# Kernel tuning notes

Hardware: AMD Instinct MI355X
Metric: run time of the kernel (lower is better)

The kernel has to match this reference:

```python
import jax, jax.numpy as jnp
import numpy as np

B, L = 64, 512          # graphs, nodes per graph
N = B * L               # total nodes
INPUT_DIM, D, H, LAYERS, OUT = 128, 128, 8, 6, 10
DH = D // H
FF = 4 * D
E = 4 * N
SCALE = 0.02


def setup_inputs() -> dict:
    key = jax.random.key(0)
    ks = jax.random.split(key, 12)
    p = {}
    p['x'] = jax.random.normal(ks[0], (N, INPUT_DIM), jnp.float32)
    p['edge_index'] = jax.random.randint(ks[1], (2, E), 0, N, dtype=jnp.int64)
    p['batch'] = jnp.repeat(jnp.arange(B, dtype=jnp.int32), L)  # sorted graph ids
    p['max_nodes'] = L
    p['Wp'] = jax.random.normal(ks[2], (INPUT_DIM, D), jnp.float32) * SCALE
    p['bp'] = jnp.zeros((D,), jnp.float32)
    p['qkv_w'] = jax.random.normal(ks[3], (LAYERS, 3 * D, D), jnp.float32) * SCALE
    p['qkv_b'] = jnp.zeros((LAYERS, 3 * D), jnp.float32)
    p['out_w'] = jax.random.normal(ks[4], (LAYERS, D, D), jnp.float32) * SCALE
    p['out_b'] = jnp.zeros((LAYERS, D), jnp.float32)
    p['ln1_g'] = jnp.ones((LAYERS, D), jnp.float32)
    p['ln1_b'] = jnp.zeros((LAYERS, D), jnp.float32)
    p['ffn_w1'] = jax.random.normal(ks[5], (LAYERS, D, FF), jnp.float32) * SCALE
    p['ffn_b1'] = jnp.zeros((LAYERS, FF), jnp.float32)
    p['ffn_w2'] = jax.random.normal(ks[6], (LAYERS, FF, D), jnp.float32) * SCALE
    p['ffn_b2'] = jnp.zeros((LAYERS, D), jnp.float32)
    p['ln2_g'] = jnp.ones((LAYERS, D), jnp.float32)
    p['ln2_b'] = jnp.zeros((LAYERS, D), jnp.float32)
    p['cls_w1'] = jax.random.normal(ks[7], (D, D // 2), jnp.float32) * SCALE
    p['cls_b1'] = jnp.zeros((D // 2,), jnp.float32)
    p['cls_w2'] = jax.random.normal(ks[8], (D // 2, OUT), jnp.float32) * SCALE
    p['cls_b2'] = jnp.zeros((OUT,), jnp.float32)
    return p


def _ln(x, g, b, eps=1e-5):
    m = x.mean(-1, keepdims=True)
    v = ((x - m) ** 2).mean(-1, keepdims=True)
    return (x - m) * jax.lax.rsqrt(v + eps) * g + b


def _forward(x, batch, max_nodes, Wp, bp, qkv_w, qkv_b, out_w, out_b,
             ln1_g, ln1_b, ffn_w1, ffn_b1, ffn_w2, ffn_b2, ln2_g, ln2_b,
             cls_w1, cls_b1, cls_w2, cls_b2):
    n = x.shape[0]
    # --- vectorized ragged-to-dense (replaces the per-graph python loop) ---
    ones = jnp.ones((n,), jnp.int32)
    counts = jax.ops.segment_sum(ones, batch, num_segments=B)          # [B]
    starts = jnp.concatenate([jnp.zeros((1,), jnp.int32), jnp.cumsum(counts)[:-1]])
    pos = jnp.arange(n, dtype=jnp.int32) - starts[batch]               # slot within graph
    h0 = x @ Wp + bp                                                   # [N, D]
    h = jnp.zeros((B, max_nodes, D), h0.dtype).at[batch, pos].set(h0)  # [B, L, D]
    mask = jnp.zeros((B, max_nodes), bool).at[batch, pos].set(True)    # [B, L]
    # additive key-padding bias (src_key_padding_mask=~mask)
    bias = jnp.where(mask, 0.0, -1e9)[:, None, None, :]                # [B,1,1,L]
    inv_sqrt = 1.0 / np.sqrt(DH)
    for i in range(LAYERS):
        # --- post-norm MHA block ---
        qkv = jnp.einsum('bld,ed->ble', h, qkv_w[i]) + qkv_b[i]        # [B,L,3D]
        q, k, v = jnp.split(qkv, 3, axis=-1)
        q = q.reshape(B, max_nodes, H, DH).transpose(0, 2, 1, 3)       # [B,H,L,dh]
        k = k.reshape(B, max_nodes, H, DH).transpose(0, 2, 1, 3)
        v = v.reshape(B, max_nodes, H, DH).transpose(0, 2, 1, 3)
        scores = jnp.einsum('bhqd,bhkd->bhqk', q, k) * inv_sqrt + bias
        attn = jax.nn.softmax(scores, axis=-1)
        o = jnp.einsum('bhqk,bhkd->bhqd', attn, v)                     # [B,H,L,dh]
        o = o.transpose(0, 2, 1, 3).reshape(B, max_nodes, D)
        o = jnp.einsum('bld,ed->ble', o, out_w[i]) + out_b[i]
        h = _ln(h + o, ln1_g[i], ln1_b[i])
        # --- FFN block ---
        ff = jax.nn.relu(h @ ffn_w1[i] + ffn_b1[i]) @ ffn_w2[i] + ffn_b2[i]
        h = _ln(h + ff, ln2_g[i], ln2_b[i])
    # --- masked mean pooling per graph ---
    denom = jnp.maximum(counts.astype(h.dtype), 1.0)[:, None]          # [B,1]
    pooled = (h * mask[..., None].astype(h.dtype)).sum(axis=1) / denom # [B,D]
    # --- classifier head ---
    hid = jax.nn.relu(pooled @ cls_w1 + cls_b1)
    return hid @ cls_w2 + cls_b2                                       # [B,OUT]


def reference(x, edge_index, batch, max_nodes, Wp, bp, qkv_w, qkv_b, out_w, out_b,
              ln1_g, ln1_b, ffn_w1, ffn_b1, ffn_w2, ffn_b2, ln2_g, ln2_b,
              cls_w1, cls_b1, cls_w2, cls_b2):
    # edge_index is accepted (as in the torch module) but never used.
    return _forward(x, batch, max_nodes, Wp, bp, qkv_w, qkv_b, out_w, out_b,
                    ln1_g, ln1_b, ffn_w1, ffn_b1, ffn_w2, ffn_b2, ln2_g, ln2_b,
                    cls_w1, cls_b1, cls_w2, cls_b2)
```

## Files before the change

kernel.cpp:

```cpp
#include <hip/hip_runtime.h>
#include <hip/hip_bf16.h>


#define NROWS (64 * 512)
#define NLAYER 6

typedef __bf16 bf16x8 __attribute__((ext_vector_type(8)));
typedef float  f32x4  __attribute__((ext_vector_type(4)));
typedef float  f32x16 __attribute__((ext_vector_type(16)));

#define QSCALE 0.36067376022224085f

#if defined(__has_builtin)
#  if __has_builtin(__builtin_amdgcn_exp2f)
#    define FAST_EXP2(x) __builtin_amdgcn_exp2f(x)
#  endif
#endif
#ifndef FAST_EXP2
#  define FAST_EXP2(x) __expf((x) * 0.6931471805599453f)
#endif

__device__ __forceinline__ __hip_bfloat16 f2bf(float x) { return __float2bfloat16(x); }

__device__ __forceinline__ __hip_bfloat16 bf_rta(float a) {
  union { float f; unsigned u; } c{a};
  return __builtin_bit_cast(__hip_bfloat16, (unsigned short)((c.u + 0x8000u) >> 16));
}
__device__ __forceinline__ unsigned pk_rta(float a, float b) {
  union { float f; unsigned u; } ca{a}, cb{b};
  return ((ca.u + 0x8000u) >> 16) | ((cb.u + 0x8000u) & 0xFFFF0000u);
}

#define PN_X   (NROWS * 128)
#define PN_WP  (128 * 128)
#define PN_QW  (6 * 384 * 128)
#define PN_QB  (6 * 384)
#define PN_OW  (6 * 128 * 128)
#define PN_W1  (6 * 128 * 512)
#define PN_W2  (6 * 512 * 128)
#define PB1 PN_X
#define PB2 (PB1 + PN_WP)
#define PB3 (PB2 + PN_QW)
#define PB4 (PB3 + PN_QB)
#define PB5 (PB4 + PN_OW)
#define PB6 (PB5 + PN_W1)
#define PB7 (PB6 + PN_W2)

__global__ __launch_bounds__(256) void prep_kernel(
    const float* __restrict__ x, __hip_bfloat16* __restrict__ xb,
    const float* __restrict__ Wp, __hip_bfloat16* __restrict__ wp_t,
    const float* __restrict__ qkv_w, __hip_bfloat16* __restrict__ qkvw,
    const float* __restrict__ qkv_b, float* __restrict__ qb_s,
    const float* __restrict__ out_w, __hip_bfloat16* __restrict__ outw,
    const float* __restrict__ ffn_w1, __hip_bfloat16* __restrict__ w1t,
    const float* __restrict__ ffn_w2, __hip_bfloat16* __restrict__ w2t)
{
  const int idx = blockIdx.x * 256 + threadIdx.x;
  if (idx < PB1) {
    xb[idx] = f2bf(x[idx]);
  } else if (idx < PB2) {
    const int i = idx - PB1;
    const int c = i >> 7, r = i & 127;
    wp_t[i] = f2bf(Wp[r * 128 + c]);
  } else if (idx < PB3) {
    const int i = idx - PB2;
    const int row = (i >> 7) % 384;
    qkvw[i] = f2bf(qkv_w[i] * ((row < 128) ? QSCALE : 1.f));
  } else if (idx < PB4) {
    const int i = idx - PB3;
    qb_s[i] = qkv_b[i] * (((i % 384) < 128) ? QSCALE : 1.f);
  } else if (idx < PB5) {
    const int i = idx - PB4;
    outw[i] = f2bf(out_w[i]);
  } else if (idx < PB6) {
    const int i = idx - PB5;
    const int l = i >> 16, j = i & 65535;
    const int c = j >> 7, r = j & 127;
    w1t[i] = f2bf(ffn_w1[l * 65536 + r * 512 + c]);
  } else if (idx < PB7) {
    const int i = idx - PB6;
    const int l = i >> 16, j = i & 65535;
    const int c = j >> 9, r = j & 511;
    w2t[i] = f2bf(ffn_w2[l * 65536 + r * 128 + c]);
  }
}

__global__ __launch_bounds__(256) void gemm_fk(
    const __hip_bfloat16* __restrict__ A, const __hip_bfloat16* __restrict__ B,
    const float* __restrict__ bias, __hip_bfloat16* __restrict__ outb,
    __hip_bfloat16* __restrict__ hb,
    const float* __restrict__ lng, const float* __restrict__ lnb,
    int M, int K, int flags)
{
  __shared__ __align__(16) __hip_bfloat16 As[64 * 136];
  __shared__ __align__(16) __hip_bfloat16 Bs[128 * 136];

  const int tid = threadIdx.x;
  const int m0 = blockIdx.x << 6;
  const int wave = tid >> 6;
  const int lane = tid & 63;
  const int quad = lane >> 4;
  const int l15 = lane & 15;
  const int wrow = wave * 16;

  f32x4 acc[8];
#pragma unroll
  for (int ni = 0; ni < 8; ++ni) acc[ni] = (f32x4){0.f, 0.f, 0.f, 0.f};

  for (int kc = 0; kc < K; kc += 128) {
#pragma unroll
    for (int p = 0; p < 4; ++p) {
      const int e = tid + (p << 8);
      const int row = e >> 4;
      const int c = e & 15;
      *(uint4*)&As[row * 136 + c * 8] =
          *(const uint4*)(A + (size_t)(m0 + row) * K + kc + c * 8);
    }
#pragma unroll
    for (int p = 0; p < 8; ++p) {
      const int e = tid + (p << 8);
      const int row = e >> 4;
      const int c = e & 15;
      *(uint4*)&Bs[row * 136 + c * 8] =
          *(const uint4*)(B + (size_t)row * K + kc + c * 8);
    }
    __syncthreads();

#pragma unroll
    for (int ks = 0; ks < 4; ++ks) {
      const bf16x8 af = *(const bf16x8*)&As[(wrow + l15) * 136 + ks * 32 + quad * 8];
#pragma unroll
      for (int ni = 0; ni < 8; ++ni) {
        const bf16x8 bfr =
            *(const bf16x8*)&Bs[(ni * 16 + l15) * 136 + ks * 32 + quad * 8];
        acc[ni] = __builtin_amdgcn_mfma_f32_16x16x32_bf16(af, bfr, acc[ni], 0, 0, 0);
      }
    }
    if (kc + 128 < K) __syncthreads();
  }

  if (flags & 2) {
#pragma unroll
    for (int r = 0; r < 4; ++r) {
      const size_t row = (size_t)(m0 + wrow + quad * 4 + r);
      float s = 0.f, sq = 0.f;
#pragma unroll
      for (int ni = 0; ni < 8; ++ni) {
        const int cl = ni * 16 + l15;
        const float v = acc[ni][r] + bias[cl] +
                        __bfloat162float(hb[row * 128 + cl]);
        acc[ni][r] = v;
        s += v;
        sq += v * v;
      }
#pragma unroll
      for (int off = 1; off <= 8; off <<= 1) {
        s += __shfl_xor(s, off, 64);
        sq += __shfl_xor(sq, off, 64);
      }
      const float mean = s * (1.f / 128.f);
      const float var = sq * (1.f / 128.f) - mean * mean;
      const float rs = rsqrtf(var + 1e-5f);
#pragma unroll
      for (int ni = 0; ni < 8; ++ni) {
        const int cl = ni * 16 + l15;
        const float o = (acc[ni][r] - mean) * rs * lng[cl] + lnb[cl];
        hb[row * 128 + cl] = bf_rta(o);
      }
    }
  } else {
#pragma unroll
    for (int ni = 0; ni < 8; ++ni) {
      const int cl = ni * 16 + l15;
      const float bv = bias[cl];
#pragma unroll
      for (int r = 0; r < 4; ++r) {
        float v = acc[ni][r] + bv;
        if (flags & 1) v = fmaxf(v, 0.f);
        outb[(size_t)(m0 + wrow + quad * 4 + r) * 128 + cl] = bf_rta(v);
      }
    }
  }
}

__global__ __launch_bounds__(256) void ffn_fused(
    __hip_bfloat16* __restrict__ hb,
    const __hip_bfloat16* __restrict__ w1,
    const __hip_bfloat16* __restrict__ w2,
    const float* __restrict__ b1, const float* __restrict__ b2,
    const float* __restrict__ lng, const float* __restrict__ lnb)
{
  __shared__ __align__(16) __hip_bfloat16 AF[64 * 136];
  __shared__ __align__(16) __hip_bfloat16 Bs[128 * 136];

  const int tid = threadIdx.x;
  const int m0 = blockIdx.x << 6;
  const int wave = tid >> 6;
  const int lane = tid & 63;
  const int quad = lane >> 4;
  const int l15 = lane & 15;
  const int wrow = wave * 16;

#pragma unroll
  for (int p = 0; p < 4; ++p) {
    const int e = tid + (p << 8);
    const int row = e >> 4, c = e & 15;
    *(uint4*)&AF[row * 136 + c * 8] =
        *(const uint4*)(hb + (size_t)(m0 + row) * 128 + c * 8);
  }
#pragma unroll
  for (int p = 0; p < 8; ++p) {
    const int e = tid + (p << 8);
    const int row = e >> 4, c = e & 15;
    *(uint4*)&Bs[row * 136 + c * 8] =
        *(const uint4*)(w1 + (size_t)row * 128 + c * 8);
  }
  __syncthreads();

  bf16x8 af[4];
#pragma unroll
  for (int ks = 0; ks < 4; ++ks)
    af[ks] = *(const bf16x8*)&AF[(wrow + l15) * 136 + ks * 32 + quad * 8];

  f32x4 oacc[8];
#pragma unroll
  for (int ni = 0; ni < 8; ++ni) oacc[ni] = (f32x4){0.f, 0.f, 0.f, 0.f};

  for (int c = 0; c < 4; ++c) {
    if (c > 0) {
      __syncthreads();
#pragma unroll
      for (int p = 0; p < 8; ++p) {
        const int e = tid + (p << 8);
        const int row = e >> 4, cc = e & 15;
        *(uint4*)&Bs[row * 136 + cc * 8] =
            *(const uint4*)(w1 + (size_t)(c * 128 + row) * 128 + cc * 8);
      }
      __syncthreads();
    }

    f32x4 fc[8];
#pragma unroll
    for (int ni = 0; ni < 8; ++ni) fc[ni] = (f32x4){0.f, 0.f, 0.f, 0.f};
#pragma unroll
    for (int ks = 0; ks < 4; ++ks)
#pragma unroll
      for (int ni = 0; ni < 8; ++ni) {
        const bf16x8 wf =
            *(const bf16x8*)&Bs[(ni * 16 + l15) * 136 + ks * 32 + quad * 8];
        fc[ni] = __builtin_amdgcn_mfma_f32_16x16x32_bf16(wf, af[ks], fc[ni], 0, 0, 0);
      }
#pragma unroll
    for (int ni = 0; ni < 8; ++ni) {
      const f32x4 bv = *(const f32x4*)(b1 + c * 128 + ni * 16 + quad * 4);
      const float v0 = fmaxf(fc[ni][0] + bv[0], 0.f);
      const float v1 = fmaxf(fc[ni][1] + bv[1], 0.f);
      const float v2 = fmaxf(fc[ni][2] + bv[2], 0.f);
      const float v3 = fmaxf(fc[ni][3] + bv[3], 0.f);
      *(uint2*)&AF[(wrow + l15) * 136 + ni * 16 + quad * 4] =
          make_uint2(pk_rta(v0, v1), pk_rta(v2, v3));
    }
    __syncthreads();

#pragma unroll
    for (int p = 0; p < 8; ++p) {
      const int e = tid + (p << 8);
      const int row = e >> 4, cc = e & 15;
      *(uint4*)&Bs[row * 136 + cc * 8] =
          *(const uint4*)(w2 + (size_t)row * 512 + c * 128 + cc * 8);
    }
    __syncthreads();

#pragma unroll
    for (int ks2 = 0; ks2 < 4; ++ks2) {
      const bf16x8 ff =
          *(const bf16x8*)&AF[(wrow + l15) * 136 + ks2 * 32 + quad * 8];
#pragma unroll
      for (int ni = 0; ni < 8; ++ni) {
        const bf16x8 wf =
            *(const bf16x8*)&Bs[(ni * 16 + l15) * 136 + ks2 * 32 + quad * 8];
        oacc[ni] = __builtin_amdgcn_mfma_f32_16x16x32_bf16(ff, wf, oacc[ni], 0, 0, 0);
      }
    }
  }

#pragma unroll
  for (int r = 0; r < 4; ++r) {
    const size_t row = (size_t)(m0 + wrow + quad * 4 + r);
    float s = 0.f, sq = 0.f;
#pragma unroll
    for (int ni = 0; ni < 8; ++ni) {
      const int cl = ni * 16 + l15;
      const float v = oacc[ni][r] + b2[cl] + __bfloat162float(hb[row * 128 + cl]);
      oacc[ni][r] = v;
      s += v;
      sq += v * v;
    }
#pragma unroll
    for (int off = 1; off <= 8; off <<= 1) {
      s += __shfl_xor(s, off, 64);
      sq += __shfl_xor(sq, off, 64);
    }
    const float mean = s * (1.f / 128.f);
    const float var = sq * (1.f / 128.f) - mean * mean;
    const float rs = rsqrtf(var + 1e-5f);
#pragma unroll
    for (int ni = 0; ni < 8; ++ni) {
      const int cl = ni * 16 + l15;
      const float o = (oacc[ni][r] - mean) * rs * lng[cl] + lnb[cl];
      hb[row * 128 + cl] = bf_rta(o);
    }
  }
}

__global__ __launch_bounds__(512) void attn_kernel(
    const __hip_bfloat16* __restrict__ hbf,
    const __hip_bfloat16* __restrict__ qkvw_l,
    const float* __restrict__ qb_l,
    __hip_bfloat16* __restrict__ o)
{
  __shared__ __align__(16) __hip_bfloat16 Ks[512 * 24];
  __shared__ __align__(16) __hip_bfloat16 Vt[16 * 520];
  __shared__ __align__(16) __hip_bfloat16 PQ[8][1536];

  const int tid = threadIdx.x;
  const int b = blockIdx.x & 63;
  const int hh = blockIdx.x >> 6;
  const __hip_bfloat16* hrow = hbf + (size_t)b * 512 * 128;

  const int wave = tid >> 6;
  const int lane = tid & 63;
  const int l31 = lane & 31;
  const int l5 = lane >> 5;
  const int l15 = lane & 15;
  const int quad = lane >> 4;
  const int q0 = wave * 64;

  {
    f32x4 qacc[4], kacc[4], vacc[4];
#pragma unroll
    for (int mt = 0; mt < 4; ++mt) {
      qacc[mt] = (f32x4){0.f, 0.f, 0.f, 0.f};
      kacc[mt] = (f32x4){0.f, 0.f, 0.f, 0.f};
      vacc[mt] = (f32x4){0.f, 0.f, 0.f, 0.f};
    }
#pragma unroll
    for (int ks = 0; ks < 4; ++ks) {
      const int kc = ks * 32 + quad * 8;
      const bf16x8 wq = *(const bf16x8*)(qkvw_l + (size_t)(hh * 16 + l15) * 128 + kc);
      const bf16x8 wk = *(const bf16x8*)(qkvw_l + (size_t)(128 + hh * 16 + l15) * 128 + kc);
      const bf16x8 wv = *(const bf16x8*)(qkvw_l + (size_t)(256 + hh * 16 + l15) * 128 + kc);
#pragma unroll
      for (int mt = 0; mt < 4; ++mt) {
        const bf16x8 hf =
            *(const bf16x8*)(hrow + (size_t)(q0 + mt * 16 + l15) * 128 + kc);
        qacc[mt] = __builtin_amdgcn_mfma_f32_16x16x32_bf16(hf, wq, qacc[mt], 0, 0, 0);
        kacc[mt] = __builtin_amdgcn_mfma_f32_16x16x32_bf16(hf, wk, kacc[mt], 0, 0, 0);
        vacc[mt] = __builtin_amdgcn_mfma_f32_16x16x32_bf16(wv, hf, vacc[mt], 0, 0, 0);
      }
    }
    const float qb = qb_l[hh * 16 + l15];
    const float kb = qb_l[128 + hh * 16 + l15];
    const f32x4 vb = *(const f32x4*)(qb_l + 256 + hh * 16 + quad * 4);
#pragma unroll
    for (int mt = 0; mt < 4; ++mt)
#pragma unroll
      for (int r = 0; r < 4; ++r) {
        const int nd = mt * 16 + quad * 4 + r;
        PQ[wave][nd * 24 + l15] = bf_rta(qacc[mt][r] + qb);
        Ks[(q0 + nd) * 24 + l15] = bf_rta(kacc[mt][r] + kb);
        Vt[(quad * 4 + r) * 520 + q0 + mt * 16 + l15] = bf_rta(vacc[mt][r] + vb[r]);
      }
  }

  bf16x8 qf[2];
#pragma unroll
  for (int s = 0; s < 2; ++s)
    qf[s] = *(const bf16x8*)&PQ[wave][(s * 32 + l31) * 24 + l5 * 8];
  __syncthreads();

  __hip_bfloat16* Pw = &PQ[wave][0];
  const f32x16 z16 = {};
  f32x4 oacc[2][2];
#pragma unroll
  for (int s = 0; s < 2; ++s) { oacc[s][0] = (f32x4){0.f,0.f,0.f,0.f};
                                oacc[s][1] = (f32x4){0.f,0.f,0.f,0.f}; }
  float lacc[2] = {0.f, 0.f};

  for (int kt = 0; kt < 16; ++kt) {
    const bf16x8 kf = *(const bf16x8*)&Ks[(kt * 32 + l31) * 24 + l5 * 8];
    const bf16x8 vf = *(const bf16x8*)&Vt[l15 * 520 + kt * 32 + quad * 8];
#pragma unroll
    for (int s = 0; s < 2; ++s) {
      f32x16 st = __builtin_amdgcn_mfma_f32_32x32x16_bf16(kf, qf[s], z16, 0, 0, 0);
      float pr[16];
#pragma unroll
      for (int r = 0; r < 16; ++r) pr[r] = FAST_EXP2(st[r]);
      const float s0 = (pr[0] + pr[1]) + (pr[2] + pr[3]);
      const float s1 = (pr[4] + pr[5]) + (pr[6] + pr[7]);
      const float s2 = (pr[8] + pr[9]) + (pr[10] + pr[11]);
      const float s3 = (pr[12] + pr[13]) + (pr[14] + pr[15]);
      lacc[s] += (s0 + s1) + (s2 + s3);
#pragma unroll
      for (int g = 0; g < 4; ++g) {
        *(uint2*)&Pw[l31 * 40 + g * 8 + l5 * 4] =
            make_uint2(pk_rta(pr[g * 4 + 0], pr[g * 4 + 1]),
                       pk_rta(pr[g * 4 + 2], pr[g * 4 + 3]));
      }
#pragma unroll
      for (int g = 0; g < 2; ++g) {
        const bf16x8 pf = *(const bf16x8*)&Pw[(g * 16 + l15) * 40 + quad * 8];
        oacc[s][g] = __builtin_amdgcn_mfma_f32_16x16x32_bf16(vf, pf, oacc[s][g], 0, 0, 0);
      }
    }
  }

#pragma unroll
  for (int s = 0; s < 2; ++s) {
    const float lv = lacc[s] + __shfl_xor(lacc[s], 32, 64);
#pragma unroll
    for (int g = 0; g < 2; ++g) {
      const float lq = __shfl(lv, g * 16 + l15, 64);
      const float inv = 1.f / lq;
      const int qrow = q0 + s * 32 + g * 16 + l15;
      *(uint2*)(o + ((size_t)b * 512 + qrow) * 128 + hh * 16 + quad * 4) =
          make_uint2(pk_rta(oacc[s][g][0] * inv, oacc[s][g][1] * inv),
                     pk_rta(oacc[s][g][2] * inv, oacc[s][g][3] * inv));
    }
  }
}

__global__ __launch_bounds__(256) void head_kernel(
    const __hip_bfloat16* __restrict__ h,
    const float* __restrict__ w1, const float* __restrict__ b1,
    const float* __restrict__ w2, const float* __restrict__ b2,
    float* __restrict__ out)
{
  __shared__ float part[2][128];
  __shared__ float pooled[128];
  __shared__ float hid[64];

  const int b = blockIdx.x;
  const int tid = threadIdx.x;
  const int d = tid & 127;
  const int half = tid >> 7;

  const __hip_bfloat16* hp = h + ((size_t)b * 512 + (size_t)half * 256) * 128;
  float s = 0.f;
  for (int r = 0; r < 256; ++r) s += __bfloat162float(hp[(size_t)r * 128 + d]);
  part[half][d] = s;
  __syncthreads();

  if (tid < 128) pooled[tid] = (part[0][tid] + part[1][tid]) * (1.f / 512.f);
  __syncthreads();

  if (tid < 64) {
    float a = b1[tid];
    for (int dd = 0; dd < 128; ++dd) a = fmaf(pooled[dd], w1[dd * 64 + tid], a);
    hid[tid] = fmaxf(a, 0.f);
  }
  __syncthreads();

  if (tid < 10) {
    float a = b2[tid];
    for (int j = 0; j < 64; ++j) a = fmaf(hid[j], w2[j * 10 + tid], a);
    out[b * 10 + tid] = a;
  }
}

extern "C" void kernel_launch(void* const* d_in, const int* in_sizes, int n_in,
                              void* d_out, int out_size, void* d_ws, size_t ws_size,
                              hipStream_t stream)
{
  (void)in_sizes; (void)n_in; (void)out_size; (void)ws_size;

  const float* x      = (const float*)d_in[0];
  const float* Wp     = (const float*)d_in[4];
  const float* bp     = (const float*)d_in[5];
  const float* qkv_w  = (const float*)d_in[6];
  const float* qkv_b  = (const float*)d_in[7];
  const float* out_w  = (const float*)d_in[8];
  const float* out_b  = (const float*)d_in[9];
  const float* ln1_g  = (const float*)d_in[10];
  const float* ln1_b  = (const float*)d_in[11];
  const float* ffn_w1 = (const float*)d_in[12];
  const float* ffn_b1 = (const float*)d_in[13];
  const float* ffn_w2 = (const float*)d_in[14];
  const float* ffn_b2 = (const float*)d_in[15];
  const float* ln2_g  = (const float*)d_in[16];
  const float* ln2_b  = (const float*)d_in[17];
  const float* cw1    = (const float*)d_in[18];
  const float* cb1    = (const float*)d_in[19];
  const float* cw2    = (const float*)d_in[20];
  const float* cb2    = (const float*)d_in[21];

  const int N = NROWS;

  __hip_bfloat16* hbf   = (__hip_bfloat16*)d_ws;
  __hip_bfloat16* xb    = hbf + (size_t)N * 128;
  __hip_bfloat16* attnb = xb + (size_t)N * 128;
  __hip_bfloat16* wp_t  = attnb + (size_t)N * 128;
  __hip_bfloat16* qkvw  = wp_t + 128 * 128;
  __hip_bfloat16* outw  = qkvw + 6 * 384 * 128;
  __hip_bfloat16* w1t   = outw + 6 * 128 * 128;
  __hip_bfloat16* w2t   = w1t + 6 * 512 * 128;
  float* qb_s = (float*)(w2t + 6 * 128 * 512);

  const dim3 blk(256);
  __hip_bfloat16* const nob = (__hip_bfloat16*)nullptr;
  const float* const nof = (const float*)nullptr;

  prep_kernel<<<dim3((PB7 + 255) / 256), blk, 0, stream>>>(
      x, xb, Wp, wp_t, qkv_w, qkvw, qkv_b, qb_s, out_w, outw,
      ffn_w1, w1t, ffn_w2, w2t);

  gemm_fk<<<dim3(N / 64), blk, 0, stream>>>(
      xb, wp_t, bp, hbf, nob, nof, nof, N, 128, 0);

  for (int i = 0; i < NLAYER; ++i) {
    attn_kernel<<<dim3(64 * 8), dim3(512), 0, stream>>>(
        hbf, qkvw + (size_t)i * 384 * 128, qb_s + (size_t)i * 384, attnb);

    gemm_fk<<<dim3(N / 64), blk, 0, stream>>>(
        attnb, outw + (size_t)i * 128 * 128, out_b + (size_t)i * 128,
        nob, hbf, ln1_g + (size_t)i * 128, ln1_b + (size_t)i * 128,
        N, 128, 2);

    ffn_fused<<<dim3(N / 64), blk, 0, stream>>>(
        hbf, w1t + (size_t)i * 512 * 128, w2t + (size_t)i * 128 * 512,
        ffn_b1 + (size_t)i * 512, ffn_b2 + (size_t)i * 128,
        ln2_g + (size_t)i * 128, ln2_b + (size_t)i * 128);
  }

  head_kernel<<<dim3(64), blk, 0, stream>>>(hbf, cw1, cb1, cw2, cb2, (float*)d_out);
}
```

Before: 511.8 us.

## Fuse out-projection+LN1 into FFN kernel and transpose MFMA operand order

Merges the attention output projection, residual add and first LayerNorm into the FFN kernel, so each layer runs one block kernel instead of two. The LN1 result stays in registers and shared memory as the FFN input and residual, which removes one global write and read of the hidden state per layer and one launch. MFMA operand order is swapped so each lane holds 4 contiguous columns of a row. That allows vectorized bias/gamma loads and packed stores in both the block kernel and the QKV projection in attention. The cost is a longer kernel with more live registers (hnew plus accumulators), which may lower occupancy.

New measurement: 600.2 us. 1.17x slower.

```diff
diff --git a/kernel.cpp b/kernel.cpp
--- a/kernel.cpp
+++ b/kernel.cpp
@@ -88,9 +88,7 @@
 __global__ __launch_bounds__(256) void gemm_fk(
     const __hip_bfloat16* __restrict__ A, const __hip_bfloat16* __restrict__ B,
     const float* __restrict__ bias, __hip_bfloat16* __restrict__ outb,
-    __hip_bfloat16* __restrict__ hb,
-    const float* __restrict__ lng, const float* __restrict__ lnb,
-    int M, int K, int flags)
+    int M, int K)
 {
   __shared__ __align__(16) __hip_bfloat16 As[64 * 136];
   __shared__ __align__(16) __hip_bfloat16 Bs[128 * 136];
@@ -139,56 +137,26 @@
     if (kc + 128 < K) __syncthreads();
   }
 
-  if (flags & 2) {
-#pragma unroll
-    for (int r = 0; r < 4; ++r) {
-      const size_t row = (size_t)(m0 + wrow + quad * 4 + r);
-      float s = 0.f, sq = 0.f;
-#pragma unroll
-      for (int ni = 0; ni < 8; ++ni) {
-        const int cl = ni * 16 + l15;
-        const float v = acc[ni][r] + bias[cl] +
-                        __bfloat162float(hb[row * 128 + cl]);
-        acc[ni][r] = v;
-        s += v;
-        sq += v * v;
-      }
-#pragma unroll
-      for (int off = 1; off <= 8; off <<= 1) {
-        s += __shfl_xor(s, off, 64);
-        sq += __shfl_xor(sq, off, 64);
-      }
-      const float mean = s * (1.f / 128.f);
-      const float var = sq * (1.f / 128.f) - mean * mean;
-      const float rs = rsqrtf(var + 1e-5f);
-#pragma unroll
-      for (int ni = 0; ni < 8; ++ni) {
-        const int cl = ni * 16 + l15;
-        const float o = (acc[ni][r] - mean) * rs * lng[cl] + lnb[cl];
-        hb[row * 128 + cl] = bf_rta(o);
-      }
-    }
-  } else {
-#pragma unroll
-    for (int ni = 0; ni < 8; ++ni) {
-      const int cl = ni * 16 + l15;
-      const float bv = bias[cl];
-#pragma unroll
-      for (int r = 0; r < 4; ++r) {
-        float v = acc[ni][r] + bv;
-        if (flags & 1) v = fmaxf(v, 0.f);
-        outb[(size_t)(m0 + wrow + quad * 4 + r) * 128 + cl] = bf_rta(v);
-      }
-    }
-  }
-}
-
-__global__ __launch_bounds__(256) void ffn_fused(
+#pragma unroll
+  for (int ni = 0; ni < 8; ++ni) {
+    const int cl = ni * 16 + l15;
+    const float bv = bias[cl];
+#pragma unroll
+    for (int r = 0; r < 4; ++r)
+      outb[(size_t)(m0 + wrow + quad * 4 + r) * 128 + cl] = bf_rta(acc[ni][r] + bv);
+  }
+}
+
+__global__ __launch_bounds__(256) void block_kernel(
+    const __hip_bfloat16* __restrict__ attnb,
     __hip_bfloat16* __restrict__ hb,
+    const __hip_bfloat16* __restrict__ outw,
+    const float* __restrict__ out_b,
+    const float* __restrict__ ln1_g, const float* __restrict__ ln1_b,
     const __hip_bfloat16* __restrict__ w1,
     const __hip_bfloat16* __restrict__ w2,
     const float* __restrict__ b1, const float* __restrict__ b2,
-    const float* __restrict__ lng, const float* __restrict__ lnb)
+    const float* __restrict__ ln2_g, const float* __restrict__ ln2_b)
 {
   __shared__ __align__(16) __hip_bfloat16 AF[64 * 136];
   __shared__ __align__(16) __hip_bfloat16 Bs[128 * 136];
@@ -199,45 +167,94 @@
   const int lane = tid & 63;
   const int quad = lane >> 4;
   const int l15 = lane & 15;
-  const int wrow = wave * 16;
+  const int lrow = wave * 16 + l15;
+  const size_t grow = (size_t)(m0 + lrow);
 
 #pragma unroll
   for (int p = 0; p < 4; ++p) {
     const int e = tid + (p << 8);
     const int row = e >> 4, c = e & 15;
     *(uint4*)&AF[row * 136 + c * 8] =
-        *(const uint4*)(hb + (size_t)(m0 + row) * 128 + c * 8);
+        *(const uint4*)(attnb + (size_t)(m0 + row) * 128 + c * 8);
   }
 #pragma unroll
   for (int p = 0; p < 8; ++p) {
     const int e = tid + (p << 8);
     const int row = e >> 4, c = e & 15;
     *(uint4*)&Bs[row * 136 + c * 8] =
-        *(const uint4*)(w1 + (size_t)row * 128 + c * 8);
+        *(const uint4*)(outw + (size_t)row * 128 + c * 8);
   }
   __syncthreads();
 
   bf16x8 af[4];
 #pragma unroll
   for (int ks = 0; ks < 4; ++ks)
-    af[ks] = *(const bf16x8*)&AF[(wrow + l15) * 136 + ks * 32 + quad * 8];
-
-  f32x4 oacc[8];
-#pragma unroll
-  for (int ni = 0; ni < 8; ++ni) oacc[ni] = (f32x4){0.f, 0.f, 0.f, 0.f};
+    af[ks] = *(const bf16x8*)&AF[lrow * 136 + ks * 32 + quad * 8];
+
+  f32x4 acc[8];
+#pragma unroll
+  for (int ni = 0; ni < 8; ++ni) acc[ni] = (f32x4){0.f, 0.f, 0.f, 0.f};
+#pragma unroll
+  for (int ks = 0; ks < 4; ++ks)
+#pragma unroll
+    for (int ni = 0; ni < 8; ++ni) {
+      const bf16x8 bfr =
+          *(const bf16x8*)&Bs[(ni * 16 + l15) * 136 + ks * 32 + quad * 8];
+      acc[ni] = __builtin_amdgcn_mfma_f32_16x16x32_bf16(bfr, af[ks], acc[ni], 0, 0, 0);
+    }
+
+  f32x4 hnew[8];
+  {
+    float s = 0.f, sq = 0.f;
+#pragma unroll
+    for (int ni = 0; ni < 8; ++ni) {
+      const f32x4 bv = *(const f32x4*)(out_b + ni * 16 + quad * 4);
+      const uint2 ru = *(const uint2*)(hb + grow * 128 + ni * 16 + quad * 4);
+      const __hip_bfloat16* rh = (const __hip_bfloat16*)&ru;
+#pragma unroll
+      for (int r = 0; r < 4; ++r) {
+        const float v = acc[ni][r] + bv[r] + __bfloat162float(rh[r]);
+        hnew[ni][r] = v;
+        s += v;
+        sq += v * v;
+      }
+    }
+    s += __shfl_xor(s, 16, 64);  sq += __shfl_xor(sq, 16, 64);
+    s += __shfl_xor(s, 32, 64);  sq += __shfl_xor(sq, 32, 64);
+    const float mean = s * (1.f / 128.f);
+    const float var = sq * (1.f / 128.f) - mean * mean;
+    const float rs = rsqrtf(var + 1e-5f);
+#pragma unroll
+    for (int ni = 0; ni < 8; ++ni) {
+      const f32x4 g4 = *(const f32x4*)(ln1_g + ni * 16 + quad * 4);
+      const f32x4 b4 = *(const f32x4*)(ln1_b + ni * 16 + quad * 4);
+      f32x4 o;
+#pragma unroll
+      for (int r = 0; r < 4; ++r) o[r] = (hnew[ni][r] - mean) * rs * g4[r] + b4[r];
+      hnew[ni] = o;
+      *(uint2*)&AF[lrow * 136 + ni * 16 + quad * 4] =
+          make_uint2(pk_rta(o[0], o[1]), pk_rta(o[2], o[3]));
+    }
+  }
+
+  bf16x8 af2[4];
+#pragma unroll
+  for (int ks = 0; ks < 4; ++ks)
+    af2[ks] = *(const bf16x8*)&AF[lrow * 136 + ks * 32 + quad * 8];
+
+#pragma unroll
+  for (int ni = 0; ni < 8; ++ni) acc[ni] = (f32x4){0.f, 0.f, 0.f, 0.f};
 
   for (int c = 0; c < 4; ++c) {
-    if (c > 0) {
-      __syncthreads();
-#pragma unroll
-      for (int p = 0; p < 8; ++p) {
-        const int e = tid + (p << 8);
-        const int row = e >> 4, cc = e & 15;
-        *(uint4*)&Bs[row * 136 + cc * 8] =
-            *(const uint4*)(w1 + (size_t)(c * 128 + row) * 128 + cc * 8);
-      }
-      __syncthreads();
-    }
+    __syncthreads();
+#pragma unroll
+    for (int p = 0; p < 8; ++p) {
+      const int e = tid + (p << 8);
+      const int row = e >> 4, cc = e & 15;
+      *(uint4*)&Bs[row * 136 + cc * 8] =
+          *(const uint4*)(w1 + (size_t)(c * 128 + row) * 128 + cc * 8);
+    }
+    __syncthreads();
 
     f32x4 fc[8];
 #pragma unroll
@@ -248,7 +265,7 @@
       for (int ni = 0; ni < 8; ++ni) {
         const bf16x8 wf =
             *(const bf16x8*)&Bs[(ni * 16 + l15) * 136 + ks * 32 + quad * 8];
-        fc[ni] = __builtin_amdgcn_mfma_f32_16x16x32_bf16(wf, af[ks], fc[ni], 0, 0, 0);
+        fc[ni] = __builtin_amdgcn_mfma_f32_16x16x32_bf16(wf, af2[ks], fc[ni], 0, 0, 0);
       }
 #pragma unroll
     for (int ni = 0; ni < 8; ++ni) {
@@ -257,11 +274,10 @@
       const float v1 = fmaxf(fc[ni][1] + bv[1], 0.f);
       const float v2 = fmaxf(fc[ni][2] + bv[2], 0.f);
       const float v3 = fmaxf(fc[ni][3] + bv[3], 0.f);
-      *(uint2*)&AF[(wrow + l15) * 136 + ni * 16 + quad * 4] =
+      *(uint2*)&AF[lrow * 136 + ni * 16 + quad * 4] =
           make_uint2(pk_rta(v0, v1), pk_rta(v2, v3));
     }
     __syncthreads();
-
 #pragma unroll
     for (int p = 0; p < 8; ++p) {
       const int e = tid + (p << 8);
@@ -273,42 +289,44 @@
 
 #pragma unroll
     for (int ks2 = 0; ks2 < 4; ++ks2) {
-      const bf16x8 ff =
-          *(const bf16x8*)&AF[(wrow + l15) * 136 + ks2 * 32 + quad * 8];
+      const bf16x8 ff = *(const bf16x8*)&AF[lrow * 136 + ks2 * 32 + quad * 8];
 #pragma unroll
       for (int ni = 0; ni < 8; ++ni) {
         const bf16x8 wf =
             *(const bf16x8*)&Bs[(ni * 16 + l15) * 136 + ks2 * 32 + quad * 8];
-        oacc[ni] = __builtin_amdgcn_mfma_f32_16x16x32_bf16(ff, wf, oacc[ni], 0, 0, 0);
-      }
-    }
-  }
-
-#pragma unroll
-  for (int r = 0; r < 4; ++r) {
-    const size_t row = (size_t)(m0 + wrow + quad * 4 + r);
+        acc[ni] = __builtin_amdgcn_mfma_f32_16x16x32_bf16(wf, ff, acc[ni], 0, 0, 0);
+      }
+    }
+  }
+
+  {
     float s = 0.f, sq = 0.f;
 #pragma unroll
     for (int ni = 0; ni < 8; ++ni) {
-      const int cl = ni * 16 + l15;
-      const float v = oacc[ni][r] + b2[cl] + __bfloat162float(hb[row * 128 + cl]);
-      oacc[ni][r] = v;
-      s += v;
-      sq += v * v;
-    }
-#pragma unroll
-    for (int off = 1; off <= 8; off <<= 1) {
-      s += __shfl_xor(s, off, 64);
-      sq += __shfl_xor(sq, off, 64);
-    }
+      const f32x4 bv = *(const f32x4*)(b2 + ni * 16 + quad * 4);
+#pragma unroll
+      for (int r = 0; r < 4; ++r) {
+        const float v = acc[ni][r] + bv[r] + hnew[ni][r];
+        acc[ni][r] = v;
+        s += v;
+        sq += v * v;
+      }
+    }
+    s += __shfl_xor(s, 16, 64);  sq += __shfl_xor(sq, 16, 64);
+    s += __shfl_xor(s, 32, 64);  sq += __shfl_xor(sq, 32, 64);
     const float mean = s * (1.f / 128.f);
     const float var = sq * (1.f / 128.f) - mean * mean;
     const float rs = rsqrtf(var + 1e-5f);
 #pragma unroll
     for (int ni = 0; ni < 8; ++ni) {
-      const int cl = ni * 16 + l15;
-      const float o = (oacc[ni][r] - mean) * rs * lng[cl] + lnb[cl];
-      hb[row * 128 + cl] = bf_rta(o);
+      const f32x4 g4 = *(const f32x4*)(ln2_g + ni * 16 + quad * 4);
+      const f32x4 b4 = *(const f32x4*)(ln2_b + ni * 16 + quad * 4);
+      const float o0 = (acc[ni][0] - mean) * rs * g4[0] + b4[0];
+      const float o1 = (acc[ni][1] - mean) * rs * g4[1] + b4[1];
+      const float o2 = (acc[ni][2] - mean) * rs * g4[2] + b4[2];
+      const float o3 = (acc[ni][3] - mean) * rs * g4[3] + b4[3];
+      *(uint2*)(hb + grow * 128 + ni * 16 + quad * 4) =
+          make_uint2(pk_rta(o0, o1), pk_rta(o2, o3));
     }
   }
 }
@@ -354,23 +372,26 @@
       for (int mt = 0; mt < 4; ++mt) {
         const bf16x8 hf =
             *(const bf16x8*)(hrow + (size_t)(q0 + mt * 16 + l15) * 128 + kc);
-        qacc[mt] = __builtin_amdgcn_mfma_f32_16x16x32_bf16(hf, wq, qacc[mt], 0, 0, 0);
-        kacc[mt] = __builtin_amdgcn_mfma_f32_16x16x32_bf16(hf, wk, kacc[mt], 0, 0, 0);
-        vacc[mt] = __builtin_amdgcn_mfma_f32_16x16x32_bf16(wv, hf, vacc[mt], 0, 0, 0);
-      }
-    }
-    const float qb = qb_l[hh * 16 + l15];
-    const float kb = qb_l[128 + hh * 16 + l15];
-    const f32x4 vb = *(const f32x4*)(qb_l + 256 + hh * 16 + quad * 4);
-#pragma unroll
-    for (int mt = 0; mt < 4; ++mt)
-#pragma unroll
-      for (int r = 0; r < 4; ++r) {
-        const int nd = mt * 16 + quad * 4 + r;
-        PQ[wave][nd * 24 + l15] = bf_rta(qacc[mt][r] + qb);
-        Ks[(q0 + nd) * 24 + l15] = bf_rta(kacc[mt][r] + kb);
-        Vt[(quad * 4 + r) * 520 + q0 + mt * 16 + l15] = bf_rta(vacc[mt][r] + vb[r]);
-      }
+        qacc[mt] = __builtin_amdgcn_mfma_f32_16x16x32_bf16(wq, hf, qacc[mt], 0, 0, 0);
+        kacc[mt] = __builtin_amdgcn_mfma_f32_16x16x32_bf16(wk, hf, kacc[mt], 0, 0, 0);
+        vacc[mt] = __builtin_amdgcn_mfma_f32_16x16x32_bf16(hf, wv, vacc[mt], 0, 0, 0);
+      }
+    }
+    const f32x4 qb4 = *(const f32x4*)(qb_l + hh * 16 + quad * 4);
+    const f32x4 kb4 = *(const f32x4*)(qb_l + 128 + hh * 16 + quad * 4);
+    const float vbs = qb_l[256 + hh * 16 + l15];
+#pragma unroll
+    for (int mt = 0; mt < 4; ++mt) {
+      *(uint2*)&PQ[wave][(mt * 16 + l15) * 24 + quad * 4] =
+          make_uint2(pk_rta(qacc[mt][0] + qb4[0], qacc[mt][1] + qb4[1]),
+                     pk_rta(qacc[mt][2] + qb4[2], qacc[mt][3] + qb4[3]));
+      *(uint2*)&Ks[(q0 + mt * 16 + l15) * 24 + quad * 4] =
+          make_uint2(pk_rta(kacc[mt][0] + kb4[0], kacc[mt][1] + kb4[1]),
+                     pk_rta(kacc[mt][2] + kb4[2], kacc[mt][3] + kb4[3]));
+      *(uint2*)&Vt[l15 * 520 + q0 + mt * 16 + quad * 4] =
+          make_uint2(pk_rta(vacc[mt][0] + vbs, vacc[mt][1] + vbs),
+                     pk_rta(vacc[mt][2] + vbs, vacc[mt][3] + vbs));
+    }
   }
 
   bf16x8 qf[2];
@@ -507,27 +528,22 @@
   float* qb_s = (float*)(w2t + 6 * 128 * 512);
 
   const dim3 blk(256);
-  __hip_bfloat16* const nob = (__hip_bfloat16*)nullptr;
-  const float* const nof = (const float*)nullptr;
 
   prep_kernel<<<dim3((PB7 + 255) / 256), blk, 0, stream>>>(
       x, xb, Wp, wp_t, qkv_w, qkvw, qkv_b, qb_s, out_w, outw,
       ffn_w1, w1t, ffn_w2, w2t);
 
-  gemm_fk<<<dim3(N / 64), blk, 0, stream>>>(
-      xb, wp_t, bp, hbf, nob, nof, nof, N, 128, 0);
+  gemm_fk<<<dim3(N / 64), blk, 0, stream>>>(xb, wp_t, bp, hbf, N, 128);
 
   for (int i = 0; i < NLAYER; ++i) {
     attn_kernel<<<dim3(64 * 8), dim3(512), 0, stream>>>(
         hbf, qkvw + (size_t)i * 384 * 128, qb_s + (size_t)i * 384, attnb);
 
-    gemm_fk<<<dim3(N / 64), blk, 0, stream>>>(
-        attnb, outw + (size_t)i * 128 * 128, out_b + (size_t)i * 128,
-        nob, hbf, ln1_g + (size_t)i * 128, ln1_b + (size_t)i * 128,
-        N, 128, 2);
-
-    ffn_fused<<<dim3(N / 64), blk, 0, stream>>>(
-        hbf, w1t + (size_t)i * 512 * 128, w2t + (size_t)i * 128 * 512,
+    block_kernel<<<dim3(N / 64), blk, 0, stream>>>(
+        attnb, hbf,
+        outw + (size_t)i * 128 * 128, out_b + (size_t)i * 128,
+        ln1_g + (size_t)i * 128, ln1_b + (size_t)i * 128,
+        w1t + (size_t)i * 512 * 128, w2t + (size_t)i * 128 * 512,
         ffn_b1 + (size_t)i * 512, ffn_b2 + (size_t)i * 128,
         ln2_g + (size_t)i * 128, ln2_b + (size_t)i * 128);
   }
```
